# Kernel optimization log

Measured on AMD Instinct MI355X. Metric: run time of the kernel, lower is better.

## Reference

```python
import jax, jax.numpy as jnp
import numpy as np

# Static graph-batch geometry: B graphs, N nodes each (contiguous), DEG avg degree.
B, N, DEG = 128, 512, 16
GID, GH = 128, 128      # g_in_dim, g_hidden_dim
CID, CE = 64, 64        # c_in_dim, c_embed_dim
HAZ = 256               # haz_dim
K1, K2, K3 = 256, 128, 64


def _gcn(x, src, dst, mask, W, b, n):
    # GCN layer with self loops over masked (surviving) nodes; masked-out nodes contribute nothing.
    h = x @ W  # [n, GH]
    w = mask[src] * mask[dst]                                  # edge alive iff both endpoints alive
    deg = mask + jax.ops.segment_sum(w, dst, num_segments=n)    # +mask = self loop
    dinv = jax.lax.rsqrt(jnp.maximum(deg, 1.0))
    norm = w * dinv[src] * dinv[dst]
    agg = jax.ops.segment_sum(norm[:, None] * h[src], dst, num_segments=n)
    self_term = h * (mask * dinv * dinv)[:, None]               # self-loop norm = 1/deg
    return (agg + self_term + b) * mask[:, None]


def _pool(x, mask, p, k):
    # Score-based top-k pooling (MVPool score -> gate -> keep top ratio per graph), mask-based for static shapes.
    score = jax.nn.sigmoid((x @ p) / jnp.sqrt(jnp.sum(p * p)))  # [B*N]
    s = jnp.where(mask > 0, score, -jnp.inf).reshape(B, N)
    _, idx = jax.lax.top_k(s, k)                                 # [B, k]
    new_mask = jnp.zeros((B, N), x.dtype).at[jnp.arange(B)[:, None], idx].set(1.0).reshape(-1)
    x = x * (score * new_mask)[:, None]
    return x, new_mask


def _readout(x, mask):
    # readout='both': concat(global_max_pool, global_mean_pool) per graph.
    xm = x.reshape(B, N, -1)
    m = mask.reshape(B, N, 1)
    mx = jnp.max(jnp.where(m > 0, xm, -1e30), axis=1)
    avg = jnp.sum(xm * m, axis=1) / jnp.maximum(jnp.sum(m, axis=1), 1.0)
    return jnp.concatenate([mx, avg], axis=1)


def _forward(x, inp_c, src, dst, W1, b1, W2, b2, W3, b3, p1, p2, p3, We, Wa, ba, Wb, bb, Wc):
    n = B * N
    mask = jnp.ones((n,), x.dtype)
    x = jax.nn.relu(_gcn(x, src, dst, mask, W1, b1, n))
    x, mask = _pool(x, mask, p1, K1)
    x1 = _readout(x, mask)
    x = jax.nn.relu(_gcn(x, src, dst, mask, W2, b2, n))
    x, mask = _pool(x, mask, p2, K2)
    x2 = _readout(x, mask)
    x = jax.nn.relu(_gcn(x, src, dst, mask, W3, b3, n))
    x, mask = _pool(x, mask, p3, K3)
    x3 = _readout(x, mask)
    hg = jax.nn.relu(x1) + jax.nn.relu(x2) + jax.nn.relu(x3)     # [B, 2*GH]
    embed = jax.nn.relu(inp_c @ We)                               # [B, CE]
    fusion = jnp.concatenate([embed, hg], axis=1)                 # [B, 320]
    h = jax.nn.relu(fusion @ Wa + ba)                             # dropout skipped (eval mode)
    h = jax.nn.relu(h @ Wb + bb)
    return h @ Wc                                                 # out_dim=1 -> Identity


def setup_inputs() -> dict:
    key = jax.random.key(0)
    ks = jax.random.split(key, 16)
    n = B * N
    x = jax.random.normal(ks[0], (n, GID), jnp.float32)
    inp_c = jax.random.normal(ks[1], (B, CID), jnp.float32)
    offs = (jnp.arange(B, dtype=jnp.int32) * N)[:, None]
    src = (jax.random.randint(ks[2], (B, N * DEG), 0, N, jnp.int32) + offs).reshape(-1)
    dst = (jax.random.randint(ks[3], (B, N * DEG), 0, N, jnp.int32) + offs).reshape(-1)
    edge_index = jnp.stack([src, dst])
    batch = jnp.arange(n, dtype=jnp.int32) // N
    def lin(k, i, o):
        return jax.random.normal(k, (i, o), jnp.float32) / np.float32(np.sqrt(i))
    return dict(
        x=x, inp_c=inp_c, edge_index=edge_index, batch=batch,
        W1=lin(ks[4], GID, GH), b1=jnp.zeros((GH,), jnp.float32),
        W2=lin(ks[5], GH, GH), b2=jnp.zeros((GH,), jnp.float32),
        W3=lin(ks[6], GH, GH), b3=jnp.zeros((GH,), jnp.float32),
        p1=jax.random.normal(ks[7], (GH,), jnp.float32),
        p2=jax.random.normal(ks[8], (GH,), jnp.float32),
        p3=jax.random.normal(ks[9], (GH,), jnp.float32),
        We=lin(ks[10], CID, CE),
        Wa=lin(ks[11], 2 * GH + CE, HAZ), ba=jnp.zeros((HAZ,), jnp.float32),
        Wb=lin(ks[12], HAZ, HAZ // 2), bb=jnp.zeros((HAZ // 2,), jnp.float32),
        Wc=lin(ks[13], HAZ // 2, 1),
    )


def reference(x, inp_c, edge_index, batch, W1, b1, W2, b2, W3, b3, p1, p2, p3, We, Wa, ba, Wb, bb, Wc):
    # batch is implicitly arange(n)//N (contiguous equal-size graphs); reductions use the reshape form.
    src, dst = edge_index[0], edge_index[1]
    return _forward(x, inp_c, src, dst, W1, b1, W2, b2, W3, b3, p1, p2, p3, We, Wa, ba, Wb, bb, Wc)
```

## Files before the change

kernel.cpp:

```cpp
#include <hip/hip_runtime.h>
#include <math.h>

#define NNODE 65536
#define NEDGE 1048576
#define NGRAPH 128
#define NPG 512
#define EPG 8192

typedef _Float16 f16x8 __attribute__((ext_vector_type(8)));
typedef _Float16 f16x4 __attribute__((ext_vector_type(4)));
typedef float f32x4 __attribute__((ext_vector_type(4)));


__global__ __launch_bounds__(512) void k_csr(const int* __restrict__ srcE, const int* __restrict__ dstE,
                                             int* __restrict__ rp, int* __restrict__ csr,
                                             float* __restrict__ gate, int* __restrict__ alive,
                                             float* __restrict__ dinv) {
    __shared__ int cnt[512];
    __shared__ int tmp[512];
    int g = blockIdx.x, t = threadIdx.x;
    int nd = g * NPG + t;
    cnt[t] = 0;
    gate[nd] = 1.f;
    alive[nd] = nd;
    __syncthreads();
    int ebase = g * EPG;
    int dl[16];
    for (int i = 0; i < 16; ++i) {
        int e = ebase + t + i * 512;
        int d = dstE[e] - g * NPG;
        dl[i] = d;
        atomicAdd(&cnt[d], 1);
    }
    __syncthreads();
    int v = cnt[t], incl = v;
    dinv[nd] = rsqrtf(1.f + (float)v);
    for (int off = 1; off < 512; off <<= 1) {
        tmp[t] = incl; __syncthreads();
        if (t >= off) incl += tmp[t - off];
        __syncthreads();
    }
    int excl = incl - v;
    rp[nd] = ebase + excl;
    if (g == NGRAPH - 1 && t == 511) rp[NNODE] = NEDGE;
    __syncthreads();
    cnt[t] = excl;
    __syncthreads();
    for (int i = 0; i < 16; ++i) {
        int e = ebase + t + i * 512;
        int pos = atomicAdd(&cnt[dl[i]], 1);
        csr[ebase + pos] = srcE[e];
    }
}


__global__ __launch_bounds__(256) void k_wconv(const float* __restrict__ W0, const float* __restrict__ W1,
                                               const float* __restrict__ W2, _Float16* __restrict__ wh,
                                               _Float16* __restrict__ wl) {
    int l = blockIdx.x >> 6;
    int e = (blockIdx.x & 63) * 256 + threadIdx.x;
    const float* W = (l == 0) ? W0 : (l == 1) ? W1 : W2;
    int k = e >> 7, n = e & 127;
    float w = W[e];
    _Float16 hi = (_Float16)w;
    _Float16 lo = (_Float16)((w - (float)hi) * 2048.0f);
    int nt = n >> 4, nn = n & 15, ks = k >> 5, quad = (k & 31) >> 3, j = k & 7;
    int off = l * 16384 + ((nt * 4 + ks) * 64 + (quad * 16 + nn)) * 8 + j;
    wh[off] = hi;
    wl[off] = lo;
}


#define CVT8(hi8, lo8, a0, a1, a2, a3, a4, a5, a6, a7)                         \
    {                                                                           \
        _Float16 q0 = (_Float16)a0, q1 = (_Float16)a1, q2 = (_Float16)a2,       \
                 q3 = (_Float16)a3, q4 = (_Float16)a4, q5 = (_Float16)a5,       \
                 q6 = (_Float16)a6, q7 = (_Float16)a7;                          \
        hi8 = (f16x8){q0, q1, q2, q3, q4, q5, q6, q7};                          \
        lo8 = (f16x8){(_Float16)((a0 - (float)q0) * 2048.f),                    \
                      (_Float16)((a1 - (float)q1) * 2048.f),                    \
                      (_Float16)((a2 - (float)q2) * 2048.f),                    \
                      (_Float16)((a3 - (float)q3) * 2048.f),                    \
                      (_Float16)((a4 - (float)q4) * 2048.f),                    \
                      (_Float16)((a5 - (float)q5) * 2048.f),                    \
                      (_Float16)((a6 - (float)q6) * 2048.f),                    \
                      (_Float16)((a7 - (float)q7) * 2048.f)};                   \
    }

__global__ __launch_bounds__(256, 2) void k_gemm(const float* __restrict__ x0, const _Float16* __restrict__ xh,
                                                 const _Float16* __restrict__ xl, const _Float16* __restrict__ wh,
                                                 const _Float16* __restrict__ wl, const float* __restrict__ gate,
                                                 const int* __restrict__ alive, float* __restrict__ h,
                                                 int srcF32, int perg) {
    __shared__ _Float16 aH[128 * 72];
    __shared__ _Float16 aL[128 * 72];
    __shared__ _Float16 bH[8192];
    __shared__ _Float16 bL[8192];
    int t = threadIdx.x;
    int lane = t & 63;
    int wv = t >> 6;
    int quad = lane >> 4, mm = lane & 15;
    int gg = blockIdx.x & 127;
    int cc0 = blockIdx.x >> 7;
    int rowbase = gg * perg + cc0 * 128;

    f32x4 accH[2][8], accM[2][8];
    for (int a = 0; a < 2; ++a)
        for (int b = 0; b < 8; ++b) {
            accH[a][b] = (f32x4){0.f, 0.f, 0.f, 0.f};
            accM[a][b] = (f32x4){0.f, 0.f, 0.f, 0.f};
        }

    for (int kh = 0; kh < 2; ++kh) {
        if (kh) __syncthreads();
        for (int pp = 0; pp < 4; ++pp) {
            int seg = t + pp * 256;
            int nt = seg >> 7, ksl = (seg >> 6) & 1, ln = seg & 63;
            int goff = ((nt * 4 + kh * 2 + ksl) * 64 + ln) * 8;
            *(uint4*)(bH + seg * 8) = *(const uint4*)(wh + goff);
            *(uint4*)(bL + seg * 8) = *(const uint4*)(wl + goff);
        }
        for (int pp = 0; pp < 4; ++pp) {
            int c = t + pp * 256;
            int r = c >> 3, ch = c & 7;
            int node = alive[rowbase + r];
            size_t src = (size_t)node * 128 + kh * 64 + ch * 8;
            f16x8 hi8, lo8;
            if (srcF32) {
                float4 v0 = *(const float4*)(x0 + src);
                float4 v1 = *(const float4*)(x0 + src + 4);
                CVT8(hi8, lo8, v0.x, v0.y, v0.z, v0.w, v1.x, v1.y, v1.z, v1.w);
            } else {
                hi8 = *(const f16x8*)(xh + src);
                lo8 = *(const f16x8*)(xl + src);
            }
            *(f16x8*)(aH + r * 72 + ch * 8) = hi8;
            *(f16x8*)(aL + r * 72 + ch * 8) = lo8;
        }
        __syncthreads();

        for (int ksl = 0; ksl < 2; ++ksl) {
            f16x8 Ah[2], Al[2];
            for (int mt = 0; mt < 2; ++mt) {
                int row = wv * 32 + mt * 16 + mm;
                Ah[mt] = *(const f16x8*)(aH + row * 72 + ksl * 32 + quad * 8);
                Al[mt] = *(const f16x8*)(aL + row * 72 + ksl * 32 + quad * 8);
            }
            for (int nt = 0; nt < 8; ++nt) {
                f16x8 Bh = *(const f16x8*)(bH + ((nt * 2 + ksl) * 64 + lane) * 8);
                f16x8 Bl = *(const f16x8*)(bL + ((nt * 2 + ksl) * 64 + lane) * 8);
                for (int mt = 0; mt < 2; ++mt) {
                    accH[mt][nt] = __builtin_amdgcn_mfma_f32_16x16x32_f16(Ah[mt], Bh, accH[mt][nt], 0, 0, 0);
                    accM[mt][nt] = __builtin_amdgcn_mfma_f32_16x16x32_f16(Ah[mt], Bl, accM[mt][nt], 0, 0, 0);
                    accM[mt][nt] = __builtin_amdgcn_mfma_f32_16x16x32_f16(Al[mt], Bh, accM[mt][nt], 0, 0, 0);
                }
            }
        }
    }

    for (int mt = 0; mt < 2; ++mt)
        for (int i = 0; i < 4; ++i) {
            int rl = wv * 32 + mt * 16 + quad * 4 + i;
            int node = alive[rowbase + rl];
            float g = gate[node];
            float* hr = h + (size_t)node * 128 + mm;
            for (int nt = 0; nt < 8; ++nt)
                hr[nt * 16] = g * (accH[mt][nt][i] + accM[mt][nt][i] * (1.f / 2048.f));
        }
}


__global__ __launch_bounds__(256) void k_agg(const float* __restrict__ h, const float* __restrict__ dinv,
                                             const int* __restrict__ rp, const int* __restrict__ csr,
                                             const int* __restrict__ alive, const float* __restrict__ bias,
                                             const float* __restrict__ p, _Float16* __restrict__ xh,
                                             _Float16* __restrict__ xl, float* __restrict__ score, int Kp) {
    __shared__ float2 nb[8][32];
    int t = threadIdx.x;
    int slot = t >> 5;
    int lane32 = t & 31;
    int half = slot & 1;
    int g = blockIdx.x & 127;
    int chunk = blockIdx.x >> 7;
    int idx = chunk * 8 + slot;

    int d = alive[g * Kp + idx];
    int jb = rp[d];
    int je = rp[d + 1];
    int deg = je - jb;

    int sid = 0; float wv = 0.f; bool livej = false;
    if (lane32 < deg) {
        sid = csr[jb + lane32];
        wv = dinv[sid];
        livej = (wv != 0.f);
    }
    unsigned long long bal = __ballot(livej);
    unsigned hm = (unsigned)(bal >> (half * 32));
    int cnt = __popc(hm);
    if (livej) {
        int pos = __popc(hm & ((1u << lane32) - 1));
        nb[slot][pos] = make_float2(wv, __int_as_float(sid));
    }

    float dvd = dinv[d];
    float4 hd = *(const float4*)(h + (size_t)d * 128 + lane32 * 4);
    float4 a0, a1, a2, a3;
    a0.x = dvd * hd.x; a0.y = dvd * hd.y; a0.z = dvd * hd.z; a0.w = dvd * hd.w;
    a1 = make_float4(0.f, 0.f, 0.f, 0.f);
    a2 = a1; a3 = a1;

    int j = 0;
    for (; j + 4 <= cnt; j += 4) {
        float2 n0 = nb[slot][j];
        float2 n1 = nb[slot][j + 1];
        float2 n2 = nb[slot][j + 2];
        float2 n3 = nb[slot][j + 3];
        float4 h0 = *(const float4*)(h + (size_t)__float_as_int(n0.y) * 128 + lane32 * 4);
        float4 h1 = *(const float4*)(h + (size_t)__float_as_int(n1.y) * 128 + lane32 * 4);
        float4 h2 = *(const float4*)(h + (size_t)__float_as_int(n2.y) * 128 + lane32 * 4);
        float4 h3 = *(const float4*)(h + (size_t)__float_as_int(n3.y) * 128 + lane32 * 4);
        a0.x = fmaf(n0.x, h0.x, a0.x); a0.y = fmaf(n0.x, h0.y, a0.y);
        a0.z = fmaf(n0.x, h0.z, a0.z); a0.w = fmaf(n0.x, h0.w, a0.w);
        a1.x = fmaf(n1.x, h1.x, a1.x); a1.y = fmaf(n1.x, h1.y, a1.y);
        a1.z = fmaf(n1.x, h1.z, a1.z); a1.w = fmaf(n1.x, h1.w, a1.w);
        a2.x = fmaf(n2.x, h2.x, a2.x); a2.y = fmaf(n2.x, h2.y, a2.y);
        a2.z = fmaf(n2.x, h2.z, a2.z); a2.w = fmaf(n2.x, h2.w, a2.w);
        a3.x = fmaf(n3.x, h3.x, a3.x); a3.y = fmaf(n3.x, h3.y, a3.y);
        a3.z = fmaf(n3.x, h3.z, a3.z); a3.w = fmaf(n3.x, h3.w, a3.w);
    }
    for (; j < cnt; ++j) {
        float2 n0 = nb[slot][j];
        float4 h0 = *(const float4*)(h + (size_t)__float_as_int(n0.y) * 128 + lane32 * 4);
        a0.x = fmaf(n0.x, h0.x, a0.x); a0.y = fmaf(n0.x, h0.y, a0.y);
        a0.z = fmaf(n0.x, h0.z, a0.z); a0.w = fmaf(n0.x, h0.w, a0.w);
    }
    for (int j2 = jb + 32; j2 < je; ++j2) {
        int s2 = csr[j2];
        float w2 = dinv[s2];
        float4 h2 = *(const float4*)(h + (size_t)s2 * 128 + lane32 * 4);
        a0.x = fmaf(w2, h2.x, a0.x); a0.y = fmaf(w2, h2.y, a0.y);
        a0.z = fmaf(w2, h2.z, a0.z); a0.w = fmaf(w2, h2.w, a0.w);
    }

    float4 b4 = *(const float4*)(bias + lane32 * 4);
    float4 o;
    o.x = fmaxf(fmaf(dvd, a0.x + a1.x + a2.x + a3.x, b4.x), 0.f);
    o.y = fmaxf(fmaf(dvd, a0.y + a1.y + a2.y + a3.y, b4.y), 0.f);
    o.z = fmaxf(fmaf(dvd, a0.z + a1.z + a2.z + a3.z, b4.z), 0.f);
    o.w = fmaxf(fmaf(dvd, a0.w + a1.w + a2.w + a3.w, b4.w), 0.f);

    _Float16 q0 = (_Float16)o.x, q1 = (_Float16)o.y, q2 = (_Float16)o.z, q3 = (_Float16)o.w;
    f16x4 oh = {q0, q1, q2, q3};
    f16x4 ol = {(_Float16)((o.x - (float)q0) * 2048.f), (_Float16)((o.y - (float)q1) * 2048.f),
                (_Float16)((o.z - (float)q2) * 2048.f), (_Float16)((o.w - (float)q3) * 2048.f)};
    *(f16x4*)(xh + (size_t)d * 128 + lane32 * 4) = oh;
    *(f16x4*)(xl + (size_t)d * 128 + lane32 * 4) = ol;

    float4 p4 = *(const float4*)(p + lane32 * 4);
    float ps = o.x * p4.x + o.y * p4.y + o.z * p4.z + o.w * p4.w;
    float q = p4.x * p4.x + p4.y * p4.y + p4.z * p4.z + p4.w * p4.w;
    for (int m = 16; m >= 1; m >>= 1) {
        ps += __shfl_xor(ps, m);
        q += __shfl_xor(q, m);
    }
    if (lane32 == 0) score[d] = 1.f / (1.f + expf(-ps * rsqrtf(q)));
}


__global__ __launch_bounds__(512) void k_pool(const _Float16* __restrict__ xh, const _Float16* __restrict__ xl,
                                              const float* __restrict__ score, float* __restrict__ gate,
                                              int* __restrict__ alive, float* __restrict__ hg,
                                              const int* __restrict__ rp, const int* __restrict__ csr,
                                              float* __restrict__ dinv, int K, int last) {
    __shared__ unsigned hist[1024];
    __shared__ unsigned wsum[8];
    __shared__ float cand[512];
    __shared__ int ad[256];
    __shared__ float ag[256];
    __shared__ float red[1024];
    __shared__ int m_new[512];
    __shared__ int scnt;
    __shared__ unsigned ccnt;
    __shared__ unsigned tbb, tbab;
    __shared__ float thrS;
    int t = threadIdx.x, g = blockIdx.x;
    int gbase = g * NPG;
    int d = gbase + t;

    float odv = dinv[d];
    int m = odv > 0.f;
    float sc = score[d];
    unsigned bits = m ? __float_as_uint(sc) : 0u;
    unsigned bucket = bits >> 21;
    hist[t] = 0; hist[t + 512] = 0;
    if (t == 0) { scnt = 0; ccnt = 0; }
    __syncthreads();
    atomicAdd(&hist[bucket], 1u);
    __syncthreads();
    unsigned a0 = hist[1023 - 2 * t];
    unsigned a1 = hist[1022 - 2 * t];
    unsigned pair = a0 + a1;
    unsigned v = pair;
    for (int o = 1; o < 64; o <<= 1) {
        unsigned n = __shfl_up(v, o);
        if ((t & 63) >= o) v += n;
    }
    if ((t & 63) == 63) wsum[t >> 6] = v;
    __syncthreads();
    if (t == 0) {
        unsigned run = 0;
        for (int i = 0; i < 8; ++i) { unsigned x = wsum[i]; wsum[i] = run; run += x; }
    }
    __syncthreads();
    unsigned incl = v + wsum[t >> 6];
    unsigned excl = incl - pair;
    unsigned uK = (unsigned)K;
    if (excl < uK && excl + a0 >= uK) { tbb = 1023 - 2 * t; tbab = excl; }
    else if (excl + a0 < uK && incl >= uK) { tbb = 1022 - 2 * t; tbab = excl + a0; }
    __syncthreads();
    unsigned bsel = tbb;
    unsigned r = uK - tbab;
    if (m && bucket == bsel) {
        unsigned pos = atomicAdd(&ccnt, 1u);
        cand[pos] = sc;
    }
    __syncthreads();
    unsigned c = ccnt;
    if (t < (int)c) {
        float vv = cand[t];
        unsigned gt = 0;
        for (unsigned i = 0; i < c; ++i) gt += (cand[i] > vv) ? 1u : 0u;
        if (gt == r - 1) thrS = vv;
    }
    __syncthreads();
    float thr = thrS;

    int nm = (m && sc >= thr) ? 1 : 0;
    gate[d] = nm ? sc : 0.f;
    m_new[t] = nm;
    if (nm) {
        int pos = atomicAdd(&scnt, 1);
        if (pos < K) {
            alive[g * K + pos] = d;
            ad[pos] = d;
            ag[pos] = sc;
        }
    }
    __syncthreads();

    if (!last) {
        float nd = 0.f;
        if (nm) {
            int jb = rp[d], je = rp[d + 1];
            int sum = 0;
            for (int j = jb; j < je; ++j) sum += m_new[csr[j] - gbase];
            nd = rsqrtf(1.f + (float)sum);
        }
        dinv[d] = nd;
    }

    int f = t & 127, c2 = t >> 7;
    float mx = 0.f, sm = 0.f;
#define REC(node) ((float)xh[(size_t)(node)*128 + f] + (float)xl[(size_t)(node)*128 + f] * (1.f / 2048.f))
    for (int j = c2; j < K; j += 16) {
        float v0 = REC(ad[j]) * ag[j];
        float v1 = REC(ad[j + 4]) * ag[j + 4];
        float v2 = REC(ad[j + 8]) * ag[j + 8];
        float v3 = REC(ad[j + 12]) * ag[j + 12];
        mx = fmaxf(fmaxf(fmaxf(mx, v0), fmaxf(v1, v2)), v3);
        sm += v0 + v1 + v2 + v3;
    }
#undef REC
    red[t] = mx; red[512 + t] = sm;
    __syncthreads();
    if (c2 == 0) {
        for (int cc = 1; cc < 4; ++cc) {
            mx = fmaxf(mx, red[cc * 128 + f]);
            sm += red[512 + cc * 128 + f];
        }
        hg[g * 256 + f] += mx;
        hg[g * 256 + 128 + f] += sm / (float)K;
    }
}


__global__ __launch_bounds__(256) void k_mlp(const float* __restrict__ inp_c, const float* __restrict__ hg,
                                             const float* __restrict__ We, const float* __restrict__ Wa,
                                             const float* __restrict__ ba, const float* __restrict__ Wb,
                                             const float* __restrict__ bb, const float* __restrict__ Wc,
                                             float* __restrict__ out) {
    __shared__ float fus[320];
    __shared__ float h1[256];
    __shared__ float h2[128];
    int t = threadIdx.x, g = blockIdx.x;
    if (t < 64) {
        float a = 0.f;
        for (int j = 0; j < 64; ++j) a = fmaf(inp_c[g * 64 + j], We[j * 64 + t], a);
        fus[t] = fmaxf(a, 0.f);
    }
    fus[64 + t] = hg[g * 256 + t];
    __syncthreads();
    {
        float a = ba[t];
        for (int j = 0; j < 320; ++j) a = fmaf(fus[j], Wa[j * 256 + t], a);
        h1[t] = fmaxf(a, 0.f);
    }
    __syncthreads();
    if (t < 128) {
        float a = bb[t];
        for (int j = 0; j < 256; ++j) a = fmaf(h1[j], Wb[j * 128 + t], a);
        h2[t] = fmaxf(a, 0.f);
    }
    __syncthreads();
    if (t == 0) {
        float a = 0.f;
        for (int j = 0; j < 128; ++j) a = fmaf(h2[j], Wc[j], a);
        out[g] = a;
    }
}


extern "C" void kernel_launch(void* const* d_in, const int* in_sizes, int n_in,
                              void* d_out, int out_size, void* d_ws, size_t ws_size,
                              hipStream_t stream) {
    (void)in_sizes; (void)n_in; (void)out_size; (void)ws_size;
    const float* x_in  = (const float*)d_in[0];
    const float* inp_c = (const float*)d_in[1];
    const int*   ei    = (const int*)d_in[2];
    const int* srcE = ei;
    const int* dstE = ei + NEDGE;
    const float* Wl[3] = {(const float*)d_in[4], (const float*)d_in[6], (const float*)d_in[8]};
    const float* bl[3] = {(const float*)d_in[5], (const float*)d_in[7], (const float*)d_in[9]};
    const float* Pl[3] = {(const float*)d_in[10], (const float*)d_in[11], (const float*)d_in[12]};
    const float* We = (const float*)d_in[13];
    const float* Wa = (const float*)d_in[14];
    const float* ba = (const float*)d_in[15];
    const float* Wb = (const float*)d_in[16];
    const float* bb = (const float*)d_in[17];
    const float* Wc = (const float*)d_in[18];
    float* out = (float*)d_out;

    char* w = (char*)d_ws;
    size_t off = 0;
    auto alloc = [&](size_t bytes) -> void* {
        void* p = w + off;
        off = (off + bytes + 255) & ~(size_t)255;
        return p;
    };
    int*   rp    = (int*)alloc((NNODE + 1) * 4);
    int*   csr   = (int*)alloc(NEDGE * 4);
    float* dinv  = (float*)alloc(NNODE * 4);
    float* gate  = (float*)alloc(NNODE * 4);
    float* score = (float*)alloc(NNODE * 4);
    int*   alive = (int*)alloc(NNODE * 4);
    float* hbuf  = (float*)alloc((size_t)NNODE * 128 * 4);
    _Float16* xh = (_Float16*)alloc((size_t)NNODE * 128 * 2);
    _Float16* xl = (_Float16*)alloc((size_t)NNODE * 128 * 2);
    float* hg    = (float*)alloc(NGRAPH * 256 * 4);
    _Float16* wfh = (_Float16*)alloc(3 * 16384 * 2);
    _Float16* wfl = (_Float16*)alloc(3 * 16384 * 2);

    hipMemsetAsync(hg, 0, NGRAPH * 256 * 4, stream);
    k_wconv<<<192, 256, 0, stream>>>(Wl[0], Wl[1], Wl[2], wfh, wfl);
    k_csr<<<NGRAPH, 512, 0, stream>>>(srcE, dstE, rp, csr, gate, alive, dinv);

    const int rows_in[3] = {65536, 32768, 16384};
    const int Ks[3] = {256, 128, 64};
    const int Kp[3] = {512, 256, 128};
    for (int l = 0; l < 3; ++l) {
        k_gemm<<<rows_in[l] / 128, 256, 0, stream>>>(x_in, xh, xl, wfh + l * 16384, wfl + l * 16384,
                                                     gate, alive, hbuf, l == 0, rows_in[l] / 128);
        k_agg<<<rows_in[l] / 8, 256, 0, stream>>>(hbuf, dinv, rp, csr, alive, bl[l], Pl[l],
                                                  xh, xl, score, Kp[l]);
        k_pool<<<NGRAPH, 512, 0, stream>>>(xh, xl, score, gate, alive, hg,
                                           rp, csr, dinv, Ks[l], l == 2);
    }
    k_mlp<<<NGRAPH, 256, 0, stream>>>(inp_c, hg, We, Wa, ba, Wb, bb, Wc, out);
}
```

Before: 286.1 us.

## Stage per-graph feature slices in LDS for neighbor aggregation

The aggregation kernel now runs one block per (graph, 64-feature half). Each block first copies that graph's 512x64 slice of h into padded shared memory, then gathers neighbor rows from LDS instead of from global memory. This assumes every edge stays inside its graph. The pooling score is split into two partial dot products that the pool kernel combines, and a new one-block kernel precomputes the projection-vector norms once. The trade-off is a very large LDS footprint, which limits each CU to one block. There are only 256 blocks, and the whole slice is loaded even in later layers where few nodes are still alive.

```diff
diff --git a/kernel.cpp b/kernel.cpp
--- a/kernel.cpp
+++ b/kernel.cpp
@@ -68,6 +68,16 @@
     int off = l * 16384 + ((nt * 4 + ks) * 64 + (quad * 16 + nn)) * 8 + j;
     wh[off] = hi;
     wl[off] = lo;
+}
+
+
+__global__ __launch_bounds__(192) void k_pnorm(const float* __restrict__ p0, const float* __restrict__ p1,
+                                               const float* __restrict__ p2, float* __restrict__ qinv) {
+    int w = threadIdx.x >> 6, lane = threadIdx.x & 63;
+    const float* P = (w == 0) ? p0 : (w == 1) ? p1 : p2;
+    float s = P[lane] * P[lane] + P[lane + 64] * P[lane + 64];
+    for (int m = 32; m >= 1; m >>= 1) s += __shfl_xor(s, m);
+    if (lane == 0) qinv[w] = rsqrtf(s);
 }
 
 
@@ -170,106 +180,105 @@
 }
 
 
-__global__ __launch_bounds__(256) void k_agg(const float* __restrict__ h, const float* __restrict__ dinv,
+__global__ __launch_bounds__(512) void k_agg(const float* __restrict__ h, const float* __restrict__ dinv,
                                              const int* __restrict__ rp, const int* __restrict__ csr,
                                              const int* __restrict__ alive, const float* __restrict__ bias,
                                              const float* __restrict__ p, _Float16* __restrict__ xh,
-                                             _Float16* __restrict__ xl, float* __restrict__ score, int Kp) {
-    __shared__ float2 nb[8][32];
+                                             _Float16* __restrict__ xl, float* __restrict__ spart, int Kp) {
+    __shared__ float hsl[512 * 68];
+    __shared__ float dinv_l[512];
+    __shared__ float2 nbw[32][16];
+    __shared__ float bias_l[64];
+    __shared__ float p_l[64];
     int t = threadIdx.x;
-    int slot = t >> 5;
-    int lane32 = t & 31;
-    int half = slot & 1;
     int g = blockIdx.x & 127;
-    int chunk = blockIdx.x >> 7;
-    int idx = chunk * 8 + slot;
-
-    int d = alive[g * Kp + idx];
-    int jb = rp[d];
-    int je = rp[d + 1];
-    int deg = je - jb;
-
-    int sid = 0; float wv = 0.f; bool livej = false;
-    if (lane32 < deg) {
-        sid = csr[jb + lane32];
-        wv = dinv[sid];
-        livej = (wv != 0.f);
-    }
-    unsigned long long bal = __ballot(livej);
-    unsigned hm = (unsigned)(bal >> (half * 32));
-    int cnt = __popc(hm);
-    if (livej) {
-        int pos = __popc(hm & ((1u << lane32) - 1));
-        nb[slot][pos] = make_float2(wv, __int_as_float(sid));
-    }
-
-    float dvd = dinv[d];
-    float4 hd = *(const float4*)(h + (size_t)d * 128 + lane32 * 4);
-    float4 a0, a1, a2, a3;
-    a0.x = dvd * hd.x; a0.y = dvd * hd.y; a0.z = dvd * hd.z; a0.w = dvd * hd.w;
-    a1 = make_float4(0.f, 0.f, 0.f, 0.f);
-    a2 = a1; a3 = a1;
-
-    int j = 0;
-    for (; j + 4 <= cnt; j += 4) {
-        float2 n0 = nb[slot][j];
-        float2 n1 = nb[slot][j + 1];
-        float2 n2 = nb[slot][j + 2];
-        float2 n3 = nb[slot][j + 3];
-        float4 h0 = *(const float4*)(h + (size_t)__float_as_int(n0.y) * 128 + lane32 * 4);
-        float4 h1 = *(const float4*)(h + (size_t)__float_as_int(n1.y) * 128 + lane32 * 4);
-        float4 h2 = *(const float4*)(h + (size_t)__float_as_int(n2.y) * 128 + lane32 * 4);
-        float4 h3 = *(const float4*)(h + (size_t)__float_as_int(n3.y) * 128 + lane32 * 4);
-        a0.x = fmaf(n0.x, h0.x, a0.x); a0.y = fmaf(n0.x, h0.y, a0.y);
-        a0.z = fmaf(n0.x, h0.z, a0.z); a0.w = fmaf(n0.x, h0.w, a0.w);
-        a1.x = fmaf(n1.x, h1.x, a1.x); a1.y = fmaf(n1.x, h1.y, a1.y);
-        a1.z = fmaf(n1.x, h1.z, a1.z); a1.w = fmaf(n1.x, h1.w, a1.w);
-        a2.x = fmaf(n2.x, h2.x, a2.x); a2.y = fmaf(n2.x, h2.y, a2.y);
-        a2.z = fmaf(n2.x, h2.z, a2.z); a2.w = fmaf(n2.x, h2.w, a2.w);
-        a3.x = fmaf(n3.x, h3.x, a3.x); a3.y = fmaf(n3.x, h3.y, a3.y);
-        a3.z = fmaf(n3.x, h3.z, a3.z); a3.w = fmaf(n3.x, h3.w, a3.w);
-    }
-    for (; j < cnt; ++j) {
-        float2 n0 = nb[slot][j];
-        float4 h0 = *(const float4*)(h + (size_t)__float_as_int(n0.y) * 128 + lane32 * 4);
-        a0.x = fmaf(n0.x, h0.x, a0.x); a0.y = fmaf(n0.x, h0.y, a0.y);
-        a0.z = fmaf(n0.x, h0.z, a0.z); a0.w = fmaf(n0.x, h0.w, a0.w);
-    }
-    for (int j2 = jb + 32; j2 < je; ++j2) {
-        int s2 = csr[j2];
-        float w2 = dinv[s2];
-        float4 h2 = *(const float4*)(h + (size_t)s2 * 128 + lane32 * 4);
-        a0.x = fmaf(w2, h2.x, a0.x); a0.y = fmaf(w2, h2.y, a0.y);
-        a0.z = fmaf(w2, h2.z, a0.z); a0.w = fmaf(w2, h2.w, a0.w);
-    }
-
-    float4 b4 = *(const float4*)(bias + lane32 * 4);
-    float4 o;
-    o.x = fmaxf(fmaf(dvd, a0.x + a1.x + a2.x + a3.x, b4.x), 0.f);
-    o.y = fmaxf(fmaf(dvd, a0.y + a1.y + a2.y + a3.y, b4.y), 0.f);
-    o.z = fmaxf(fmaf(dvd, a0.z + a1.z + a2.z + a3.z, b4.z), 0.f);
-    o.w = fmaxf(fmaf(dvd, a0.w + a1.w + a2.w + a3.w, b4.w), 0.f);
-
-    _Float16 q0 = (_Float16)o.x, q1 = (_Float16)o.y, q2 = (_Float16)o.z, q3 = (_Float16)o.w;
-    f16x4 oh = {q0, q1, q2, q3};
-    f16x4 ol = {(_Float16)((o.x - (float)q0) * 2048.f), (_Float16)((o.y - (float)q1) * 2048.f),
-                (_Float16)((o.z - (float)q2) * 2048.f), (_Float16)((o.w - (float)q3) * 2048.f)};
-    *(f16x4*)(xh + (size_t)d * 128 + lane32 * 4) = oh;
-    *(f16x4*)(xl + (size_t)d * 128 + lane32 * 4) = ol;
-
-    float4 p4 = *(const float4*)(p + lane32 * 4);
-    float ps = o.x * p4.x + o.y * p4.y + o.z * p4.z + o.w * p4.w;
-    float q = p4.x * p4.x + p4.y * p4.y + p4.z * p4.z + p4.w * p4.w;
-    for (int m = 16; m >= 1; m >>= 1) {
-        ps += __shfl_xor(ps, m);
-        q += __shfl_xor(q, m);
-    }
-    if (lane32 == 0) score[d] = 1.f / (1.f + expf(-ps * rsqrtf(q)));
+    int fh = blockIdx.x >> 7;
+    int fb = fh * 64;
+    int gbase = g * NPG;
+
+    for (int r0 = 0; r0 < 512; r0 += 64) {
+        int r = r0 + (t >> 3);
+        int f8 = (t & 7) * 8;
+        const float* src = h + (size_t)(gbase + r) * 128 + fb + f8;
+        float4 v0 = *(const float4*)(src);
+        float4 v1 = *(const float4*)(src + 4);
+        *(float4*)(hsl + r * 68 + f8) = v0;
+        *(float4*)(hsl + r * 68 + f8 + 4) = v1;
+    }
+    dinv_l[t] = dinv[gbase + t];
+    if (t < 64) { bias_l[t] = bias[fb + t]; p_l[t] = p[fb + t]; }
+    __syncthreads();
+
+    int lane16 = t & 15;
+    int qid = t >> 4;
+
+    for (int idx = qid; idx < Kp; idx += 32) {
+        int d = alive[g * Kp + idx];
+        int rd = d - gbase;
+        int jb = rp[d], je = rp[d + 1];
+        float dvd = dinv_l[rd];
+        float4 hd = *(const float4*)(hsl + rd * 68 + lane16 * 4);
+        float4 acc;
+        acc.x = dvd * hd.x; acc.y = dvd * hd.y; acc.z = dvd * hd.z; acc.w = dvd * hd.w;
+
+        for (int bk = jb; bk < je; bk += 16) {
+            int nk = je - bk; if (nk > 16) nk = 16;
+            float wv = 0.f;
+            int rs = rd;
+            if (lane16 < nk) {
+                rs = csr[bk + lane16] - gbase;
+                wv = dinv_l[rs];
+            }
+            nbw[qid][lane16] = make_float2(wv, __int_as_float(rs));
+            int nk4 = (nk + 3) & ~3;
+            for (int k = 0; k < nk4; k += 4) {
+                float2 e0 = nbw[qid][k];
+                float2 e1 = nbw[qid][k + 1];
+                float2 e2 = nbw[qid][k + 2];
+                float2 e3 = nbw[qid][k + 3];
+                float4 h0 = *(const float4*)(hsl + __float_as_int(e0.y) * 68 + lane16 * 4);
+                float4 h1 = *(const float4*)(hsl + __float_as_int(e1.y) * 68 + lane16 * 4);
+                float4 h2 = *(const float4*)(hsl + __float_as_int(e2.y) * 68 + lane16 * 4);
+                float4 h3 = *(const float4*)(hsl + __float_as_int(e3.y) * 68 + lane16 * 4);
+                acc.x = fmaf(e0.x, h0.x, acc.x); acc.y = fmaf(e0.x, h0.y, acc.y);
+                acc.z = fmaf(e0.x, h0.z, acc.z); acc.w = fmaf(e0.x, h0.w, acc.w);
+                acc.x = fmaf(e1.x, h1.x, acc.x); acc.y = fmaf(e1.x, h1.y, acc.y);
+                acc.z = fmaf(e1.x, h1.z, acc.z); acc.w = fmaf(e1.x, h1.w, acc.w);
+                acc.x = fmaf(e2.x, h2.x, acc.x); acc.y = fmaf(e2.x, h2.y, acc.y);
+                acc.z = fmaf(e2.x, h2.z, acc.z); acc.w = fmaf(e2.x, h2.w, acc.w);
+                acc.x = fmaf(e3.x, h3.x, acc.x); acc.y = fmaf(e3.x, h3.y, acc.y);
+                acc.z = fmaf(e3.x, h3.z, acc.z); acc.w = fmaf(e3.x, h3.w, acc.w);
+            }
+        }
+
+        float4 b4 = *(const float4*)(bias_l + lane16 * 4);
+        float4 o;
+        o.x = fmaxf(fmaf(dvd, acc.x, b4.x), 0.f);
+        o.y = fmaxf(fmaf(dvd, acc.y, b4.y), 0.f);
+        o.z = fmaxf(fmaf(dvd, acc.z, b4.z), 0.f);
+        o.w = fmaxf(fmaf(dvd, acc.w, b4.w), 0.f);
+
+        _Float16 q0 = (_Float16)o.x, q1 = (_Float16)o.y, q2 = (_Float16)o.z, q3 = (_Float16)o.w;
+        f16x4 oh = {q0, q1, q2, q3};
+        f16x4 ol = {(_Float16)((o.x - (float)q0) * 2048.f), (_Float16)((o.y - (float)q1) * 2048.f),
+                    (_Float16)((o.z - (float)q2) * 2048.f), (_Float16)((o.w - (float)q3) * 2048.f)};
+        *(f16x4*)(xh + (size_t)d * 128 + fb + lane16 * 4) = oh;
+        *(f16x4*)(xl + (size_t)d * 128 + fb + lane16 * 4) = ol;
+
+        float4 p4 = *(const float4*)(p_l + lane16 * 4);
+        float ps = o.x * p4.x + o.y * p4.y + o.z * p4.z + o.w * p4.w;
+        ps += __shfl_xor(ps, 1);
+        ps += __shfl_xor(ps, 2);
+        ps += __shfl_xor(ps, 4);
+        ps += __shfl_xor(ps, 8);
+        if (lane16 == 0) spart[(size_t)fh * NNODE + d] = ps;
+    }
 }
 
 
 __global__ __launch_bounds__(512) void k_pool(const _Float16* __restrict__ xh, const _Float16* __restrict__ xl,
-                                              const float* __restrict__ score, float* __restrict__ gate,
+                                              const float* __restrict__ spart, const float* __restrict__ qinv,
+                                              int lidx, float* __restrict__ gate,
                                               int* __restrict__ alive, float* __restrict__ hg,
                                               const int* __restrict__ rp, const int* __restrict__ csr,
                                               float* __restrict__ dinv, int K, int last) {
@@ -290,7 +299,8 @@
 
     float odv = dinv[d];
     int m = odv > 0.f;
-    float sc = score[d];
+    float z = spart[d] + spart[NNODE + d];
+    float sc = 1.f / (1.f + expf(-z * qinv[lidx]));
     unsigned bits = m ? __float_as_uint(sc) : 0u;
     unsigned bucket = bits >> 21;
     hist[t] = 0; hist[t + 512] = 0;
@@ -452,7 +462,8 @@
     int*   csr   = (int*)alloc(NEDGE * 4);
     float* dinv  = (float*)alloc(NNODE * 4);
     float* gate  = (float*)alloc(NNODE * 4);
-    float* score = (float*)alloc(NNODE * 4);
+    float* spart = (float*)alloc((size_t)2 * NNODE * 4);
+    float* qinv  = (float*)alloc(256);
     int*   alive = (int*)alloc(NNODE * 4);
     float* hbuf  = (float*)alloc((size_t)NNODE * 128 * 4);
     _Float16* xh = (_Float16*)alloc((size_t)NNODE * 128 * 2);
@@ -463,6 +474,7 @@
 
     hipMemsetAsync(hg, 0, NGRAPH * 256 * 4, stream);
     k_wconv<<<192, 256, 0, stream>>>(Wl[0], Wl[1], Wl[2], wfh, wfl);
+    k_pnorm<<<1, 192, 0, stream>>>(Pl[0], Pl[1], Pl[2], qinv);
     k_csr<<<NGRAPH, 512, 0, stream>>>(srcE, dstE, rp, csr, gate, alive, dinv);
 
     const int rows_in[3] = {65536, 32768, 16384};
@@ -471,9 +483,9 @@
     for (int l = 0; l < 3; ++l) {
         k_gemm<<<rows_in[l] / 128, 256, 0, stream>>>(x_in, xh, xl, wfh + l * 16384, wfl + l * 16384,
                                                      gate, alive, hbuf, l == 0, rows_in[l] / 128);
-        k_agg<<<rows_in[l] / 8, 256, 0, stream>>>(hbuf, dinv, rp, csr, alive, bl[l], Pl[l],
-                                                  xh, xl, score, Kp[l]);
-        k_pool<<<NGRAPH, 512, 0, stream>>>(xh, xl, score, gate, alive, hg,
+        k_agg<<<256, 512, 0, stream>>>(hbuf, dinv, rp, csr, alive, bl[l], Pl[l],
+                                       xh, xl, spart, Kp[l]);
+        k_pool<<<NGRAPH, 512, 0, stream>>>(xh, xl, spart, qinv, l, gate, alive, hg,
                                            rp, csr, dinv, Ks[l], l == 2);
     }
     k_mlp<<<NGRAPH, 256, 0, stream>>>(inp_c, hg, We, Wa, ba, Wb, bb, Wc, out);
```

Result: slower. 298.9 us (+4.5%).
